# Performance work log

Measured on AMD Instinct MI355X. Metric: run time of the kernel, lower is better.

Reference implementation:

```python
import jax, jax.numpy as jnp
import numpy as np

N_NODES = 20000
N_EDGES = 160000
N_CONFIG = 1000
OP_SIZE = 120
OP_FEATURE = 140
CONFIG_FEATURE = 24
HID = 256
EMB = 128


def _mynorm(x, axis):
    # InstanceNorm1d (affine=False): biased var, eps=1e-5, normalized over `axis`
    m = jnp.mean(x, axis=axis, keepdims=True)
    v = jnp.var(x, axis=axis, keepdims=True)
    return (x - m) / jnp.sqrt(v + 1e-5)


def _gelu(x):
    return jax.nn.gelu(x, approximate=False)


def _segment_softmax(e, seg, num):
    m = jax.ops.segment_max(e, seg, num_segments=num)
    ex = jnp.exp(e - m[seg])
    s = jax.ops.segment_sum(ex, seg, num_segments=num)
    return ex / (s[seg] + 1e-16)


def setup_inputs() -> dict:
    key = jax.random.key(0)
    ks = jax.random.split(key, 24)
    d = {}
    d['node_feat'] = jax.random.normal(ks[0], (N_NODES, OP_FEATURE), jnp.float32)
    d['config_feat'] = jax.random.normal(ks[1], (N_CONFIG, CONFIG_FEATURE), jnp.float32)
    d['node_feat_mean'] = jax.random.normal(ks[2], (OP_FEATURE,), jnp.float32)
    d['node_feat_std'] = jax.random.uniform(ks[3], (OP_FEATURE,), jnp.float32)
    d['config_feat_mean'] = jax.random.normal(ks[4], (CONFIG_FEATURE,), jnp.float32)
    d['config_feat_std'] = jax.random.uniform(ks[5], (CONFIG_FEATURE,), jnp.float32)
    d['embed_table'] = jax.random.normal(ks[6], (OP_SIZE, EMB), jnp.float32)
    d['early_W1'] = jax.random.normal(ks[7], (EMB + OP_FEATURE, HID), jnp.float32) * 0.05
    d['early_W2'] = jax.random.normal(ks[8], (HID, HID), jnp.float32) * 0.05
    d['gat_Wl'] = jax.random.normal(ks[9], (4, HID, HID), jnp.float32) * 0.05
    d['gat_bl'] = jax.random.normal(ks[10], (4, HID), jnp.float32) * 0.05
    d['gat_Wr'] = jax.random.normal(ks[11], (4, HID, HID), jnp.float32) * 0.05
    d['gat_br'] = jax.random.normal(ks[12], (4, HID), jnp.float32) * 0.05
    d['gat_att'] = jax.random.normal(ks[13], (4, HID), jnp.float32) * 0.05
    d['gat_bias'] = jax.random.normal(ks[14], (4, HID), jnp.float32) * 0.05
    d['late_W1'] = jax.random.normal(ks[15], (HID + CONFIG_FEATURE, HID), jnp.float32) * 0.05
    d['late_W2'] = jax.random.normal(ks[16], (HID, HID // 2), jnp.float32) * 0.05
    d['pred_W'] = jax.random.normal(ks[17], (HID // 2, 1), jnp.float32) * 0.05
    d['pred_b'] = jax.random.normal(ks[18], (1,), jnp.float32) * 0.05
    d['node_opcode'] = jax.random.randint(ks[19], (N_NODES,), 0, OP_SIZE, jnp.int64)
    d['edge_index'] = jax.random.randint(ks[20], (2, N_EDGES), 0, N_NODES, jnp.int64)
    return d


def reference(node_feat, config_feat, node_feat_mean, node_feat_std,
              config_feat_mean, config_feat_std, embed_table,
              early_W1, early_W2, gat_Wl, gat_bl, gat_Wr, gat_br,
              gat_att, gat_bias, late_W1, late_W2, pred_W, pred_b,
              node_opcode, edge_index):
    N = node_feat.shape[0]
    # embedding with max_norm=1: renormalize looked-up rows to L2 norm <= 1
    emb = embed_table[node_opcode]
    nrm = jnp.sqrt(jnp.sum(emb * emb, axis=-1, keepdims=True))
    emb = emb * jnp.minimum(1.0, 1.0 / (nrm + 1e-7))
    feat = (node_feat - node_feat_mean) / (node_feat_std + 1e-4)
    x = jnp.concatenate([emb, feat], axis=-1)  # [N, 268]
    # early MLP (norm over node axis per channel)
    x = _gelu(_mynorm(x @ early_W1, 0))
    x = _gelu(_mynorm(x @ early_W2, 0))
    # add self loops (PyG GATv2Conv default)
    loop = jnp.arange(N, dtype=edge_index.dtype)
    src = jnp.concatenate([edge_index[0], loop])  # message source j
    dst = jnp.concatenate([edge_index[1], loop])  # message target i
    for i in range(4):
        xl = x @ gat_Wl[i] + gat_bl[i]
        xr = x @ gat_Wr[i] + gat_br[i]
        h = xl[src] + xr[dst]                      # [E+N, HID]
        e = jax.nn.leaky_relu(h, 0.2) @ gat_att[i]  # [E+N]
        alpha = _segment_softmax(e, dst, N)
        out = jax.ops.segment_sum(alpha[:, None] * xl[src], dst, num_segments=N)
        out = out + gat_bias[i]
        x = _gelu(_mynorm(out, 0))
    pool = jnp.mean(x, axis=0) + jnp.max(x, axis=0)  # [HID]
    cf = (config_feat - config_feat_mean) / (config_feat_std + 1e-4)
    C = cf.shape[0]
    x_late = jnp.concatenate([cf, jnp.broadcast_to(pool, (C, pool.shape[0]))], axis=1)
    h = _gelu(_mynorm(x_late @ late_W1, 0))  # 2D MyNorm1d normalizes over batch axis
    h = _gelu(_mynorm(h @ late_W2, 0))
    runtime = (h @ pred_W + pred_b)[:, 0]
    return runtime
```

## Files before the change

### kernel.cpp

```cpp
#include <hip/hip_runtime.h>
#include <math.h>

#define N_NODES 20000
#define N_EDGES 160000
#define N_CFG   1000
#define OP_FEAT 140
#define CFG_FEAT 24
#define HID     256
#define EMB     128
#define E_TOT   (N_EDGES + N_NODES)
#define K288    288
#define MPAD    20096
#define NW      512

typedef __attribute__((ext_vector_type(8))) short short8v;
typedef __attribute__((ext_vector_type(4))) float f32x4;

__device__ __forceinline__ short f2bf(float f) {
  unsigned u = __float_as_uint(f);
  unsigned r = (u + 0x7FFFu + ((u >> 16) & 1u)) >> 16;
  return (short)r;
}
__device__ __forceinline__ float bf2f(short s) {
  return __uint_as_float(((unsigned)(unsigned short)s) << 16);
}
__device__ __forceinline__ float gelu_f(float x) {
  return 0.5f * x * (1.0f + erff(x * 0.70710678118654752f));
}

#define GLOAD_LDS(gptr, lptr) __builtin_amdgcn_global_load_lds( \
    (const __attribute__((address_space(1))) void*)(gptr),      \
    (__attribute__((address_space(3))) void*)(lptr), 16, 0, 0)

__global__ void prep_weights(
    const float* __restrict__ eW1, const float* __restrict__ eW2,
    const float* __restrict__ lW1, const float* __restrict__ lW2,
    const float* __restrict__ Wl, const float* __restrict__ Wr,
    const float* __restrict__ bl, const float* __restrict__ br,
    short* __restrict__ W1t, short* __restrict__ W2t,
    short* __restrict__ lW1t, short* __restrict__ lW2t,
    short* __restrict__ Wlrt, float* __restrict__ blr)
{
  int i = blockIdx.x * 256 + threadIdx.x;
  const int s1 = HID * K288;
  const int s2 = HID * HID;
  const int s3 = HID * K288;
  const int s4 = 128 * HID;
  const int s5 = 4 * NW * HID;
  const int s6 = 4 * NW;
  if (i < s1) { int n = i / K288, k = i % K288;
    W1t[i] = (k < EMB + OP_FEAT) ? f2bf(eW1[(size_t)k * HID + n]) : (short)0; return; }
  i -= s1;
  if (i < s2) { int n = i >> 8, k = i & 255;
    W2t[i] = f2bf(eW2[(size_t)k * HID + n]); return; }
  i -= s2;
  if (i < s3) { int n = i / K288, k = i % K288;
    lW1t[i] = (k < CFG_FEAT + HID) ? f2bf(lW1[(size_t)k * HID + n]) : (short)0; return; }
  i -= s3;
  if (i < s4) { int n = i >> 8, k = i & 255;
    lW2t[i] = f2bf(lW2[(size_t)k * 128 + n]); return; }
  i -= s4;
  if (i < s5) { int l = i >> 17, rem = i & 131071, n = rem >> 8, k = rem & 255;
    float v = (n < HID) ? Wl[(size_t)l * HID * HID + (size_t)k * HID + n]
                        : Wr[(size_t)l * HID * HID + (size_t)k * HID + (n - HID)];
    Wlrt[i] = f2bf(v); return; }
  i -= s5;
  if (i < s6) { int l = i >> 9, j = i & 511;
    blr[i] = (j < HID) ? bl[l * HID + j] : br[l * HID + j - HID]; }
}

__global__ __launch_bounds__(256) void prep_kernel(
    const float* __restrict__ node_feat, const float* __restrict__ nf_mean,
    const float* __restrict__ nf_std, const float* __restrict__ emb_table,
    const int* __restrict__ opcode, short* __restrict__ x268b)
{
  int wave = threadIdx.x >> 6;
  int lane = threadIdx.x & 63;
  int row = blockIdx.x * 4 + wave;
  if (row >= N_NODES) return;
  int op = opcode[row];
  float t0 = emb_table[op * EMB + lane];
  float t1 = emb_table[op * EMB + 64 + lane];
  float ss = t0 * t0 + t1 * t1;
  #pragma unroll
  for (int off = 32; off; off >>= 1) ss += __shfl_xor(ss, off);
  float sc = fminf(1.0f, 1.0f / (sqrtf(ss) + 1e-7f));
  short* dst = x268b + (size_t)row * K288;
  dst[lane] = f2bf(t0 * sc);
  dst[64 + lane] = f2bf(t1 * sc);
  for (int k = lane; k < OP_FEAT; k += 64)
    dst[EMB + k] = f2bf((node_feat[(size_t)row * OP_FEAT + k] - nf_mean[k]) / (nf_std[k] + 1e-4f));
  if (lane < K288 - EMB - OP_FEAT) dst[EMB + OP_FEAT + lane] = 0;
}

__global__ __launch_bounds__(256) void gemm_mfma(
    const short* __restrict__ A, const short* __restrict__ Wt,
    const float* __restrict__ bias, float* __restrict__ C,
    short* __restrict__ Cb, float* __restrict__ stats,
    int M, int N, int Kpad)
{
  __shared__ __align__(16) short As[2][4][128][8];
  __shared__ __align__(16) short Bs[2][4][128][8];
  int tid = threadIdx.x;
  int wave = tid >> 6, lane = tid & 63;
  int bm = blockIdx.x * 128, bn = blockIdx.y * 128;
  int wr = (wave >> 1) * 64, wc = (wave & 1) * 64;
  int g = lane >> 4, r16 = lane & 15;
  f32x4 acc[4][4] = {};
  int nt = Kpad >> 5;

  int sA = wave * 2;
  auto STAGE = [&](int t, int b) {
    int k0 = t * 32;
    #pragma unroll
    for (int s2 = 0; s2 < 2; s2++) {
      int s = sA + s2;
      int sg = s >> 1, r0 = (s & 1) * 64;
      GLOAD_LDS(A  + (size_t)(bm + r0 + lane) * Kpad + k0 + sg * 8, &As[b][sg][r0][0]);
      GLOAD_LDS(Wt + (size_t)(bn + r0 + lane) * Kpad + k0 + sg * 8, &Bs[b][sg][r0][0]);
    }
  };

  STAGE(0, 0);
  for (int t = 0; t < nt; t++) {
    int b = t & 1;
    __syncthreads();
    if (t + 1 < nt) STAGE(t + 1, b ^ 1);
    short8v af[4], bfv[4];
    #pragma unroll
    for (int mi = 0; mi < 4; mi++)
      af[mi] = *(const short8v*)&As[b][g][wr + mi * 16 + r16][0];
    #pragma unroll
    for (int ni = 0; ni < 4; ni++)
      bfv[ni] = *(const short8v*)&Bs[b][g][wc + ni * 16 + r16][0];
    #pragma unroll
    for (int mi = 0; mi < 4; mi++)
      #pragma unroll
      for (int ni = 0; ni < 4; ni++)
        acc[mi][ni] = __builtin_amdgcn_mfma_f32_16x16x32_bf16(af[mi], bfv[ni], acc[mi][ni], 0, 0, 0);
  }

  int rg = lane >> 4;
  #pragma unroll
  for (int ni = 0; ni < 4; ni++) {
    int gc = bn + wc + ni * 16 + r16;
    float bv = bias ? bias[gc] : 0.f;
    float s = 0.f, sq = 0.f;
    #pragma unroll
    for (int mi = 0; mi < 4; mi++) {
      #pragma unroll
      for (int r = 0; r < 4; r++) {
        int gr = bm + wr + mi * 16 + rg * 4 + r;
        if (gr < M) {
          float v = acc[mi][ni][r] + bv;
          if (C)  C[(size_t)gr * N + gc] = v;
          if (Cb) Cb[(size_t)gr * N + gc] = f2bf(v);
          s += v; sq += v * v;
        }
      }
    }
    if (stats) {
      s  += __shfl_xor(s, 16);  sq += __shfl_xor(sq, 16);
      s  += __shfl_xor(s, 32);  sq += __shfl_xor(sq, 32);
      if (rg == 0) { atomicAdd(&stats[gc], s); atomicAdd(&stats[N + gc], sq); }
    }
  }
}

__global__ void colstats(const float* __restrict__ X, int M, int C,
                         float* __restrict__ stats)
{
  int c = threadIdx.x;
  int r0 = blockIdx.x * 64;
  int r1 = min(r0 + 64, M);
  float s = 0.f, sq = 0.f;
  for (int r = r0; r < r1; r++) {
    float v = X[(size_t)r * C + c];
    s += v; sq += v * v;
  }
  atomicAdd(&stats[c], s);
  atomicAdd(&stats[C + c], sq);
}

__global__ void norm_gelu(const float* __restrict__ X, short* __restrict__ Yb,
                          int M, int C, const float* __restrict__ stats)
{
  int i4 = blockIdx.x * blockDim.x + threadIdx.x;
  int idx = i4 * 4;
  if (idx >= M * C) return;
  int c = idx & (C - 1);
  float invM = 1.0f / (float)M;
  f32x4 x = *(const f32x4*)(X + idx);
  short4 y;
  #pragma unroll
  for (int j = 0; j < 4; j++) {
    float mean = stats[c + j] * invM;
    float var = stats[C + c + j] * invM - mean * mean;
    float v = gelu_f((x[j] - mean) * rsqrtf(var + 1e-5f));
    ((short*)&y)[j] = f2bf(v);
  }
  *(short4*)(Yb + idx) = y;
}

__global__ void edge_count(const int* __restrict__ ei, int* __restrict__ counts) {
  int e = blockIdx.x * blockDim.x + threadIdx.x;
  if (e >= E_TOT) return;
  int dst = (e < N_EDGES) ? ei[N_EDGES + e] : (e - N_EDGES);
  atomicAdd(&counts[dst], 1);
}

__global__ __launch_bounds__(1024) void scan_kernel(const int* __restrict__ counts,
                                                    int* __restrict__ indptr)
{
  __shared__ int sh[1024];
  int t = threadIdx.x;
  const int chunk = (N_NODES + 1023) / 1024;
  int start = t * chunk, end = min(start + chunk, N_NODES);
  int sum = 0;
  for (int i = start; i < end; i++) sum += counts[i];
  sh[t] = sum;
  __syncthreads();
  for (int off = 1; off < 1024; off <<= 1) {
    int v = (t >= off) ? sh[t - off] : 0;
    __syncthreads();
    sh[t] += v;
    __syncthreads();
  }
  int run = (t > 0) ? sh[t - 1] : 0;
  for (int i = start; i < end; i++) { indptr[i] = run; run += counts[i]; }
  if (t == 1023) indptr[N_NODES] = run;
}

__global__ void edge_fill(const int* __restrict__ ei, const int* __restrict__ indptr,
                          int* __restrict__ cursor, int* __restrict__ col)
{
  int e = blockIdx.x * blockDim.x + threadIdx.x;
  if (e >= E_TOT) return;
  int src, dst;
  if (e < N_EDGES) { src = ei[e]; dst = ei[N_EDGES + e]; }
  else             { src = dst = e - N_EDGES; }
  int pos = indptr[dst] + atomicAdd(&cursor[dst], 1);
  col[pos] = src;
}

__global__ __launch_bounds__(256) void gat_agg(
    const short* __restrict__ xlr,
    const int* __restrict__ indptr, const int* __restrict__ col,
    const float* __restrict__ att, const float* __restrict__ bias,
    float* __restrict__ out)
{
  int wave = threadIdx.x >> 6, lane = threadIdx.x & 63;
  int node = blockIdx.x * 4 + wave;
  if (node >= N_NODES) return;
  float attc[4], xri[4], o[4] = {0, 0, 0, 0};
  {
    short4 xr4 = *(const short4*)(xlr + (size_t)node * NW + HID + lane * 4);
    #pragma unroll
    for (int k = 0; k < 4; k++) {
      attc[k] = att[lane * 4 + k];
      xri[k] = bf2f(((short*)&xr4)[k]);
    }
  }
  float m = -INFINITY, s = 0.f;
  int e0 = indptr[node], e1 = indptr[node + 1];
  for (int e = e0; e < e1; e++) {
    int j = col[e];
    short4 xl4 = *(const short4*)(xlr + (size_t)j * NW + lane * 4);
    float xlj[4], p = 0.f;
    #pragma unroll
    for (int k = 0; k < 4; k++) {
      xlj[k] = bf2f(((short*)&xl4)[k]);
      float h = xlj[k] + xri[k];
      float lr = h > 0.f ? h : 0.2f * h;
      p += lr * attc[k];
    }
    #pragma unroll
    for (int off = 32; off; off >>= 1) p += __shfl_xor(p, off);
    float mn = fmaxf(m, p);
    float scale = __expf(m - mn);
    float w = __expf(p - mn);
    s = s * scale + w;
    #pragma unroll
    for (int k = 0; k < 4; k++) o[k] = o[k] * scale + w * xlj[k];
    m = mn;
  }
  float inv = 1.0f / (s + 1e-16f);
  f32x4 ov;
  #pragma unroll
  for (int k = 0; k < 4; k++) ov[k] = o[k] * inv + bias[lane * 4 + k];
  *(f32x4*)(out + (size_t)node * HID + lane * 4) = ov;
}

__device__ __forceinline__ unsigned fenc(float f) {
  unsigned b = __float_as_uint(f);
  return (b & 0x80000000u) ? ~b : (b | 0x80000000u);
}
__device__ __forceinline__ float fdec(unsigned u) {
  unsigned b = (u & 0x80000000u) ? (u & 0x7FFFFFFFu) : ~u;
  return __uint_as_float(b);
}

__global__ void pool_reduce(const short* __restrict__ Xb, float* __restrict__ psum,
                            unsigned* __restrict__ pmax)
{
  int c = threadIdx.x;
  int r0 = blockIdx.x * 64, r1 = min(r0 + 64, N_NODES);
  float s = 0.f, mx = -INFINITY;
  for (int r = r0; r < r1; r++) {
    float v = bf2f(Xb[(size_t)r * HID + c]);
    s += v; mx = fmaxf(mx, v);
  }
  atomicAdd(&psum[c], s);
  atomicMax(&pmax[c], fenc(mx));
}

__global__ void build_xlate(const float* __restrict__ cfg, const float* __restrict__ cmean,
                            const float* __restrict__ cstd, const float* __restrict__ psum,
                            const unsigned* __restrict__ pmax, short* __restrict__ xlateb)
{
  int i = blockIdx.x * blockDim.x + threadIdx.x;
  if (i >= N_CFG * K288) return;
  int r = i / K288, c = i % K288;
  float v;
  if (c < CFG_FEAT) v = (cfg[r * CFG_FEAT + c] - cmean[c]) / (cstd[c] + 1e-4f);
  else if (c < CFG_FEAT + HID) {
    int p = c - CFG_FEAT;
    v = psum[p] * (1.0f / N_NODES) + fdec(pmax[p]);
  } else v = 0.f;
  xlateb[i] = f2bf(v);
}

__global__ __launch_bounds__(64) void pred_kernel(
    const float* __restrict__ h2, const float* __restrict__ stats,
    const float* __restrict__ W, const float* __restrict__ b,
    float* __restrict__ out)
{
  int r = blockIdx.x, lane = threadIdx.x;
  const float invM = 1.0f / (float)N_CFG;
  float v = 0.f;
  #pragma unroll
  for (int t = 0; t < 2; t++) {
    int c = lane + 64 * t;
    float mean = stats[c] * invM;
    float var = stats[128 + c] * invM - mean * mean;
    float y = gelu_f((h2[(size_t)r * 128 + c] - mean) * rsqrtf(var + 1e-5f));
    v += y * W[c];
  }
  #pragma unroll
  for (int off = 32; off; off >>= 1) v += __shfl_xor(v, off);
  if (lane == 0) out[r] = v + b[0];
}

extern "C" void kernel_launch(void* const* d_in, const int* in_sizes, int n_in,
                              void* d_out, int out_size, void* d_ws, size_t ws_size,
                              hipStream_t stream)
{
  const float* node_feat   = (const float*)d_in[0];
  const float* config_feat = (const float*)d_in[1];
  const float* nf_mean     = (const float*)d_in[2];
  const float* nf_std      = (const float*)d_in[3];
  const float* cf_mean     = (const float*)d_in[4];
  const float* cf_std      = (const float*)d_in[5];
  const float* emb_table   = (const float*)d_in[6];
  const float* early_W1    = (const float*)d_in[7];
  const float* early_W2    = (const float*)d_in[8];
  const float* gat_Wl      = (const float*)d_in[9];
  const float* gat_bl      = (const float*)d_in[10];
  const float* gat_Wr      = (const float*)d_in[11];
  const float* gat_br      = (const float*)d_in[12];
  const float* gat_att     = (const float*)d_in[13];
  const float* gat_bias    = (const float*)d_in[14];
  const float* late_W1     = (const float*)d_in[15];
  const float* late_W2     = (const float*)d_in[16];
  const float* pred_W      = (const float*)d_in[17];
  const float* pred_b      = (const float*)d_in[18];
  const int*   node_opcode = (const int*)d_in[19];
  const int*   edge_index  = (const int*)d_in[20];
  float* out = (float*)d_out;
  (void)in_sizes; (void)n_in; (void)out_size; (void)ws_size;

  char* ws = (char*)d_ws;
  size_t off = 0;
  auto alloc = [&](size_t bytes) -> void* {
    void* p = ws + off;
    off += (bytes + 255) & ~255ull;
    return p;
  };
  short* x268b = (short*)alloc((size_t)MPAD * K288 * 2);
  float* bufB  = (float*)alloc((size_t)N_NODES * HID * 4);
  short* bufAb = (short*)alloc((size_t)MPAD * HID * 2);
  short* xlr   = (short*)alloc((size_t)N_NODES * NW * 2);
  int* indptr  = (int*)alloc((N_NODES + 1) * 4);
  int* colidx  = (int*)alloc((size_t)E_TOT * 4);
  short* xlateb = (short*)alloc((size_t)1024 * K288 * 2);
  float* h1    = (float*)alloc((size_t)N_CFG * HID * 4);
  short* h1b   = (short*)alloc((size_t)1024 * HID * 2);
  float* h2    = (float*)alloc((size_t)N_CFG * 128 * 4);
  short* W1t   = (short*)alloc((size_t)HID * K288 * 2);
  short* W2t   = (short*)alloc((size_t)HID * HID * 2);
  short* Wlrt  = (short*)alloc((size_t)4 * NW * HID * 2);
  float* blr   = (float*)alloc(4 * NW * 4);
  short* lW1t  = (short*)alloc((size_t)HID * K288 * 2);
  short* lW2t  = (short*)alloc((size_t)128 * HID * 2);

  float* zbase = (float*)alloc((8 * 1024 + 512 + 2 * N_NODES) * 4);
  float* stats8 = zbase;
  float* psum   = zbase + 8192;
  unsigned* pmax = (unsigned*)(zbase + 8192 + 256);
  int* counts   = (int*)(zbase + 8192 + 512);
  int* cursor   = counts + N_NODES;
  const size_t zbytes = (8 * 1024 + 512 + 2 * N_NODES) * 4;
  auto slot = [&](int s) { return stats8 + s * 1024; };

  auto run_gemm = [&](const short* A, const short* Wt, const float* bias, float* C,
                      short* Cb, float* stats, int M, int N, int Kpad) {
    dim3 grid((M + 127) / 128, N / 128);
    hipLaunchKernelGGL(gemm_mfma, grid, dim3(256), 0, stream, A, Wt, bias, C, Cb, stats,
                       M, N, Kpad);
  };

  hipMemsetAsync(zbase, 0, zbytes, stream);

  {
    int total = HID * K288 + HID * HID + HID * K288 + 128 * HID + 4 * NW * HID + 4 * NW;
    hipLaunchKernelGGL(prep_weights, dim3((total + 255) / 256), dim3(256), 0, stream,
                       early_W1, early_W2, late_W1, late_W2, gat_Wl, gat_Wr, gat_bl, gat_br,
                       W1t, W2t, lW1t, lW2t, Wlrt, blr);
  }

  hipLaunchKernelGGL(edge_count, dim3((E_TOT + 255) / 256), dim3(256), 0, stream,
                     edge_index, counts);
  hipLaunchKernelGGL(scan_kernel, dim3(1), dim3(1024), 0, stream, counts, indptr);
  hipLaunchKernelGGL(edge_fill, dim3((E_TOT + 255) / 256), dim3(256), 0, stream,
                     edge_index, indptr, cursor, colidx);

  hipLaunchKernelGGL(prep_kernel, dim3((N_NODES + 3) / 4), dim3(256), 0, stream,
                     node_feat, nf_mean, nf_std, emb_table, node_opcode, x268b);
  run_gemm(x268b, W1t, nullptr, bufB, nullptr, slot(0), N_NODES, HID, K288);
  hipLaunchKernelGGL(norm_gelu, dim3((N_NODES * HID / 4 + 255) / 256), dim3(256), 0, stream,
                     bufB, bufAb, N_NODES, HID, slot(0));
  run_gemm(bufAb, W2t, nullptr, bufB, nullptr, slot(1), N_NODES, HID, HID);
  hipLaunchKernelGGL(norm_gelu, dim3((N_NODES * HID / 4 + 255) / 256), dim3(256), 0, stream,
                     bufB, bufAb, N_NODES, HID, slot(1));

  for (int l = 0; l < 4; l++) {
    run_gemm(bufAb, Wlrt + (size_t)l * NW * HID, blr + l * NW, nullptr, xlr, nullptr,
             N_NODES, NW, HID);
    hipLaunchKernelGGL(gat_agg, dim3((N_NODES + 3) / 4), dim3(256), 0, stream,
                       xlr, indptr, colidx, gat_att + l * HID, gat_bias + l * HID, bufB);
    hipLaunchKernelGGL(colstats, dim3((N_NODES + 63) / 64), dim3(HID), 0, stream,
                       bufB, N_NODES, HID, slot(2 + l));
    hipLaunchKernelGGL(norm_gelu, dim3((N_NODES * HID / 4 + 255) / 256), dim3(256), 0, stream,
                       bufB, bufAb, N_NODES, HID, slot(2 + l));
  }

  hipLaunchKernelGGL(pool_reduce, dim3((N_NODES + 63) / 64), dim3(HID), 0, stream,
                     bufAb, psum, pmax);

  hipLaunchKernelGGL(build_xlate, dim3((N_CFG * K288 + 255) / 256), dim3(256), 0, stream,
                     config_feat, cf_mean, cf_std, psum, pmax, xlateb);
  run_gemm(xlateb, lW1t, nullptr, h1, nullptr, slot(6), N_CFG, HID, K288);
  hipLaunchKernelGGL(norm_gelu, dim3((N_CFG * HID / 4 + 255) / 256), dim3(256), 0, stream,
                     h1, h1b, N_CFG, HID, slot(6));
  run_gemm(h1b, lW2t, nullptr, h2, nullptr, slot(7), N_CFG, 128, HID);
  hipLaunchKernelGGL(pred_kernel, dim3(N_CFG), dim3(64), 0, stream,
                     h2, slot(7), pred_W, pred_b, out);
}
```

Baseline: 605.7 us.

## Fuse column stats into GAT aggregation, fold pooling into norm, add BM=64 GEMM

```diff
diff --git a/kernel.cpp b/kernel.cpp
--- a/kernel.cpp
+++ b/kernel.cpp
@@ -93,31 +93,42 @@
   if (lane < K288 - EMB - OP_FEAT) dst[EMB + OP_FEAT + lane] = 0;
 }
 
+template<int BM>
 __global__ __launch_bounds__(256) void gemm_mfma(
     const short* __restrict__ A, const short* __restrict__ Wt,
     const float* __restrict__ bias, float* __restrict__ C,
     short* __restrict__ Cb, float* __restrict__ stats,
     int M, int N, int Kpad)
 {
-  __shared__ __align__(16) short As[2][4][128][8];
+  constexpr int MI = (BM == 128) ? 4 : 2;
+  __shared__ __align__(16) short As[2][4][BM][8];
   __shared__ __align__(16) short Bs[2][4][128][8];
   int tid = threadIdx.x;
   int wave = tid >> 6, lane = tid & 63;
-  int bm = blockIdx.x * 128, bn = blockIdx.y * 128;
-  int wr = (wave >> 1) * 64, wc = (wave & 1) * 64;
+  int bm = blockIdx.x * BM, bn = blockIdx.y * 128;
+  int wr = (BM == 128) ? (wave >> 1) * 64 : (wave & 1) * 32;
+  int wc = (BM == 128) ? (wave & 1) * 64 : (wave >> 1) * 64;
   int g = lane >> 4, r16 = lane & 15;
-  f32x4 acc[4][4] = {};
+  f32x4 acc[MI][4] = {};
   int nt = Kpad >> 5;
 
-  int sA = wave * 2;
   auto STAGE = [&](int t, int b) {
     int k0 = t * 32;
-    #pragma unroll
-    for (int s2 = 0; s2 < 2; s2++) {
-      int s = sA + s2;
-      int sg = s >> 1, r0 = (s & 1) * 64;
-      GLOAD_LDS(A  + (size_t)(bm + r0 + lane) * Kpad + k0 + sg * 8, &As[b][sg][r0][0]);
-      GLOAD_LDS(Wt + (size_t)(bn + r0 + lane) * Kpad + k0 + sg * 8, &Bs[b][sg][r0][0]);
+    if constexpr (BM == 128) {
+      #pragma unroll
+      for (int s2 = 0; s2 < 2; s2++) {
+        int s = wave * 2 + s2;
+        int sg = s >> 1, r0 = (s & 1) * 64;
+        GLOAD_LDS(A  + (size_t)(bm + r0 + lane) * Kpad + k0 + sg * 8, &As[b][sg][r0][0]);
+        GLOAD_LDS(Wt + (size_t)(bn + r0 + lane) * Kpad + k0 + sg * 8, &Bs[b][sg][r0][0]);
+      }
+    } else {
+      GLOAD_LDS(A + (size_t)(bm + lane) * Kpad + k0 + wave * 8, &As[b][wave][0][0]);
+      #pragma unroll
+      for (int s2 = 0; s2 < 2; s2++) {
+        int sg = s2 * 2 + (wave >> 1), r0 = (wave & 1) * 64;
+        GLOAD_LDS(Wt + (size_t)(bn + r0 + lane) * Kpad + k0 + sg * 8, &Bs[b][sg][r0][0]);
+      }
     }
   };
 
@@ -126,15 +137,15 @@
     int b = t & 1;
     __syncthreads();
     if (t + 1 < nt) STAGE(t + 1, b ^ 1);
-    short8v af[4], bfv[4];
-    #pragma unroll
-    for (int mi = 0; mi < 4; mi++)
+    short8v af[MI], bfv[4];
+    #pragma unroll
+    for (int mi = 0; mi < MI; mi++)
       af[mi] = *(const short8v*)&As[b][g][wr + mi * 16 + r16][0];
     #pragma unroll
     for (int ni = 0; ni < 4; ni++)
       bfv[ni] = *(const short8v*)&Bs[b][g][wc + ni * 16 + r16][0];
     #pragma unroll
-    for (int mi = 0; mi < 4; mi++)
+    for (int mi = 0; mi < MI; mi++)
       #pragma unroll
       for (int ni = 0; ni < 4; ni++)
         acc[mi][ni] = __builtin_amdgcn_mfma_f32_16x16x32_bf16(af[mi], bfv[ni], acc[mi][ni], 0, 0, 0);
@@ -147,7 +158,7 @@
     float bv = bias ? bias[gc] : 0.f;
     float s = 0.f, sq = 0.f;
     #pragma unroll
-    for (int mi = 0; mi < 4; mi++) {
+    for (int mi = 0; mi < MI; mi++) {
       #pragma unroll
       for (int r = 0; r < 4; r++) {
         int gr = bm + wr + mi * 16 + rg * 4 + r;
@@ -167,39 +178,28 @@
   }
 }
 
-__global__ void colstats(const float* __restrict__ X, int M, int C,
-                         float* __restrict__ stats)
+__global__ void norm_gelu_col(const float* __restrict__ X, short* __restrict__ Yb,
+                              int M, int C, const float* __restrict__ stats,
+                              float* __restrict__ psum, unsigned* __restrict__ pmax)
 {
   int c = threadIdx.x;
-  int r0 = blockIdx.x * 64;
-  int r1 = min(r0 + 64, M);
-  float s = 0.f, sq = 0.f;
+  int r0 = blockIdx.x * 32, r1 = min(r0 + 32, M);
+  float invM = 1.0f / (float)M;
+  float mean = stats[c] * invM;
+  float var = stats[C + c] * invM - mean * mean;
+  float inv = rsqrtf(var + 1e-5f);
+  float s = 0.f, mx = -INFINITY;
   for (int r = r0; r < r1; r++) {
-    float v = X[(size_t)r * C + c];
-    s += v; sq += v * v;
-  }
-  atomicAdd(&stats[c], s);
-  atomicAdd(&stats[C + c], sq);
-}
-
-__global__ void norm_gelu(const float* __restrict__ X, short* __restrict__ Yb,
-                          int M, int C, const float* __restrict__ stats)
-{
-  int i4 = blockIdx.x * blockDim.x + threadIdx.x;
-  int idx = i4 * 4;
-  if (idx >= M * C) return;
-  int c = idx & (C - 1);
-  float invM = 1.0f / (float)M;
-  f32x4 x = *(const f32x4*)(X + idx);
-  short4 y;
-  #pragma unroll
-  for (int j = 0; j < 4; j++) {
-    float mean = stats[c + j] * invM;
-    float var = stats[C + c + j] * invM - mean * mean;
-    float v = gelu_f((x[j] - mean) * rsqrtf(var + 1e-5f));
-    ((short*)&y)[j] = f2bf(v);
-  }
-  *(short4*)(Yb + idx) = y;
+    float y = gelu_f((X[(size_t)r * C + c] - mean) * inv);
+    Yb[(size_t)r * C + c] = f2bf(y);
+    s += y; mx = fmaxf(mx, y);
+  }
+  if (psum) {
+    unsigned b = __float_as_uint(mx);
+    unsigned enc = (b & 0x80000000u) ? ~b : (b | 0x80000000u);
+    atomicAdd(&psum[c], s);
+    atomicMax(&pmax[c], enc);
+  }
 }
 
 __global__ void edge_count(const int* __restrict__ ei, int* __restrict__ counts) {
@@ -243,15 +243,19 @@
   col[pos] = src;
 }
 
-__global__ __launch_bounds__(256) void gat_agg(
+__global__ __launch_bounds__(1024) void gat_agg(
     const short* __restrict__ xlr,
     const int* __restrict__ indptr, const int* __restrict__ col,
     const float* __restrict__ att, const float* __restrict__ bias,
-    float* __restrict__ out)
-{
-  int wave = threadIdx.x >> 6, lane = threadIdx.x & 63;
-  int node = blockIdx.x * 4 + wave;
-  if (node >= N_NODES) return;
+    float* __restrict__ out, float* __restrict__ stats)
+{
+  __shared__ float sums[HID];
+  __shared__ float sqs[HID];
+  int tid = threadIdx.x;
+  if (tid < HID) { sums[tid] = 0.f; sqs[tid] = 0.f; }
+  __syncthreads();
+  int wave = tid >> 6, lane = tid & 63;
+  int node = blockIdx.x * 16 + wave;
   float attc[4], xri[4], o[4] = {0, 0, 0, 0};
   {
     short4 xr4 = *(const short4*)(xlr + (size_t)node * NW + HID + lane * 4);
@@ -287,31 +291,23 @@
   float inv = 1.0f / (s + 1e-16f);
   f32x4 ov;
   #pragma unroll
-  for (int k = 0; k < 4; k++) ov[k] = o[k] * inv + bias[lane * 4 + k];
+  for (int k = 0; k < 4; k++) {
+    float v = o[k] * inv + bias[lane * 4 + k];
+    ov[k] = v;
+    atomicAdd(&sums[lane * 4 + k], v);
+    atomicAdd(&sqs[lane * 4 + k], v * v);
+  }
   *(f32x4*)(out + (size_t)node * HID + lane * 4) = ov;
-}
-
-__device__ __forceinline__ unsigned fenc(float f) {
-  unsigned b = __float_as_uint(f);
-  return (b & 0x80000000u) ? ~b : (b | 0x80000000u);
-}
+  __syncthreads();
+  if (tid < HID) {
+    atomicAdd(&stats[tid], sums[tid]);
+    atomicAdd(&stats[HID + tid], sqs[tid]);
+  }
+}
+
 __device__ __forceinline__ float fdec(unsigned u) {
   unsigned b = (u & 0x80000000u) ? (u & 0x7FFFFFFFu) : ~u;
   return __uint_as_float(b);
-}
-
-__global__ void pool_reduce(const short* __restrict__ Xb, float* __restrict__ psum,
-                            unsigned* __restrict__ pmax)
-{
-  int c = threadIdx.x;
-  int r0 = blockIdx.x * 64, r1 = min(r0 + 64, N_NODES);
-  float s = 0.f, mx = -INFINITY;
-  for (int r = r0; r < r1; r++) {
-    float v = bf2f(Xb[(size_t)r * HID + c]);
-    s += v; mx = fmaxf(mx, v);
-  }
-  atomicAdd(&psum[c], s);
-  atomicMax(&pmax[c], fenc(mx));
 }
 
 __global__ void build_xlate(const float* __restrict__ cfg, const float* __restrict__ cmean,
@@ -412,11 +408,18 @@
   const size_t zbytes = (8 * 1024 + 512 + 2 * N_NODES) * 4;
   auto slot = [&](int s) { return stats8 + s * 1024; };
 
-  auto run_gemm = [&](const short* A, const short* Wt, const float* bias, float* C,
+  auto run_gemm = [&](int BM, const short* A, const short* Wt, const float* bias, float* C,
                       short* Cb, float* stats, int M, int N, int Kpad) {
-    dim3 grid((M + 127) / 128, N / 128);
-    hipLaunchKernelGGL(gemm_mfma, grid, dim3(256), 0, stream, A, Wt, bias, C, Cb, stats,
-                       M, N, Kpad);
+    dim3 grid((M + BM - 1) / BM, N / 128);
+    if (BM == 128)
+      hipLaunchKernelGGL(gemm_mfma<128>, grid, dim3(256), 0, stream, A, Wt, bias, C, Cb, stats, M, N, Kpad);
+    else
+      hipLaunchKernelGGL(gemm_mfma<64>, grid, dim3(256), 0, stream, A, Wt, bias, C, Cb, stats, M, N, Kpad);
+  };
+  auto run_norm = [&](const float* X, short* Yb, int M, int C, float* stats,
+                      float* ps, unsigned* pm) {
+    hipLaunchKernelGGL(norm_gelu_col, dim3((M + 31) / 32), dim3(C), 0, stream,
+                       X, Yb, M, C, stats, ps, pm);
   };
 
   hipMemsetAsync(zbase, 0, zbytes, stream);
@@ -436,33 +439,26 @@
 
   hipLaunchKernelGGL(prep_kernel, dim3((N_NODES + 3) / 4), dim3(256), 0, stream,
                      node_feat, nf_mean, nf_std, emb_table, node_opcode, x268b);
-  run_gemm(x268b, W1t, nullptr, bufB, nullptr, slot(0), N_NODES, HID, K288);
-  hipLaunchKernelGGL(norm_gelu, dim3((N_NODES * HID / 4 + 255) / 256), dim3(256), 0, stream,
-                     bufB, bufAb, N_NODES, HID, slot(0));
-  run_gemm(bufAb, W2t, nullptr, bufB, nullptr, slot(1), N_NODES, HID, HID);
-  hipLaunchKernelGGL(norm_gelu, dim3((N_NODES * HID / 4 + 255) / 256), dim3(256), 0, stream,
-                     bufB, bufAb, N_NODES, HID, slot(1));
+  run_gemm(64, x268b, W1t, nullptr, bufB, nullptr, slot(0), N_NODES, HID, K288);
+  run_norm(bufB, bufAb, N_NODES, HID, slot(0), nullptr, nullptr);
+  run_gemm(64, bufAb, W2t, nullptr, bufB, nullptr, slot(1), N_NODES, HID, HID);
+  run_norm(bufB, bufAb, N_NODES, HID, slot(1), nullptr, nullptr);
 
   for (int l = 0; l < 4; l++) {
-    run_gemm(bufAb, Wlrt + (size_t)l * NW * HID, blr + l * NW, nullptr, xlr, nullptr,
+    run_gemm(128, bufAb, Wlrt + (size_t)l * NW * HID, blr + l * NW, nullptr, xlr, nullptr,
              N_NODES, NW, HID);
-    hipLaunchKernelGGL(gat_agg, dim3((N_NODES + 3) / 4), dim3(256), 0, stream,
-                       xlr, indptr, colidx, gat_att + l * HID, gat_bias + l * HID, bufB);
-    hipLaunchKernelGGL(colstats, dim3((N_NODES + 63) / 64), dim3(HID), 0, stream,
-                       bufB, N_NODES, HID, slot(2 + l));
-    hipLaunchKernelGGL(norm_gelu, dim3((N_NODES * HID / 4 + 255) / 256), dim3(256), 0, stream,
-                       bufB, bufAb, N_NODES, HID, slot(2 + l));
-  }
-
-  hipLaunchKernelGGL(pool_reduce, dim3((N_NODES + 63) / 64), dim3(HID), 0, stream,
-                     bufAb, psum, pmax);
+    hipLaunchKernelGGL(gat_agg, dim3(N_NODES / 16), dim3(1024), 0, stream,
+                       xlr, indptr, colidx, gat_att + l * HID, gat_bias + l * HID,
+                       bufB, slot(2 + l));
+    run_norm(bufB, bufAb, N_NODES, HID, slot(2 + l),
+             (l == 3) ? psum : nullptr, (l == 3) ? pmax : nullptr);
+  }
 
   hipLaunchKernelGGL(build_xlate, dim3((N_CFG * K288 + 255) / 256), dim3(256), 0, stream,
                      config_feat, cf_mean, cf_std, psum, pmax, xlateb);
-  run_gemm(xlateb, lW1t, nullptr, h1, nullptr, slot(6), N_CFG, HID, K288);
-  hipLaunchKernelGGL(norm_gelu, dim3((N_CFG * HID / 4 + 255) / 256), dim3(256), 0, stream,
-                     h1, h1b, N_CFG, HID, slot(6));
-  run_gemm(h1b, lW2t, nullptr, h2, nullptr, slot(7), N_CFG, 128, HID);
+  run_gemm(64, xlateb, lW1t, nullptr, h1, nullptr, slot(6), N_CFG, HID, K288);
+  run_norm(h1, h1b, N_CFG, HID, slot(6), nullptr, nullptr);
+  run_gemm(64, h1b, lW2t, nullptr, h2, nullptr, slot(7), N_CFG, 128, HID);
   hipLaunchKernelGGL(pred_kernel, dim3(N_CFG), dim3(64), 0, stream,
                      h2, slot(7), pred_W, pred_b, out);
 }
```

After: 757.7 us. 1.25x slower.
